# Kernel tuning notes

Hardware: AMD Instinct MI355X
Metric: run time of the kernel (lower is better)

## Reference

```python
import jax, jax.numpy as jnp
import numpy as np
import math

# config constants (from init_kwargs)
W_ROSE, W_QUALITY, W_VOLUME = 0.5, 0.3, 0.2
EPS = 1e-8
DEGEN_EPS = 1e-8


def _rose_score(v):
    # v: [N, n, d] -> [N]; centroid-based radial cosine rose score
    n = v.shape[-2]
    centroid = v.mean(axis=-2, keepdims=True)
    radial = v - centroid
    norms = jnp.clip(jnp.linalg.norm(radial, axis=-1, keepdims=True), EPS)
    u = radial / norms
    cos = jnp.einsum('...id,...jd->...ij', u, u)            # [N, n, n]
    diag = jnp.einsum('...ii->...', cos)
    cos_mean = (cos.sum(axis=(-1, -2)) - diag) / (n * (n - 1))  # off-diagonal mean
    return (cos_mean + 1.0) * 0.5


def _pairwise_sq_dists(v):
    diff = v[..., :, None, :] - v[..., None, :, :]
    return jnp.sum(diff * diff, axis=-1)                    # [N, n, n]


def _regularity(v):
    # SimplexQuality regularity: min_edge / max_edge (1.0 for a regular simplex)
    n = v.shape[-2]
    d = jnp.sqrt(jnp.clip(_pairwise_sq_dists(v), 1e-12))
    off = ~np.eye(n, dtype=bool)                            # static boolean mask
    edges = d[..., off]                                     # [N, n*(n-1)]
    return edges.min(axis=-1) / jnp.clip(edges.max(axis=-1), EPS)


def _cayley_menger_volume(v):
    # v: [N, n, d]; k-simplex with k = n-1; Cayley-Menger determinant volume
    n = v.shape[-2]
    k = n - 1
    d2 = _pairwise_sq_dists(v)                              # [N, n, n]
    bs = d2.shape[:-2]
    top = jnp.concatenate([jnp.zeros(bs + (1, 1), d2.dtype),
                           jnp.ones(bs + (1, n), d2.dtype)], axis=-1)
    bot = jnp.concatenate([jnp.ones(bs + (n, 1), d2.dtype), d2], axis=-1)
    cm = jnp.concatenate([top, bot], axis=-2)               # [N, n+1, n+1]
    det = jnp.linalg.det(cm)
    coeff = ((-1.0) ** (k + 1)) / (2.0 ** k * float(math.factorial(k)) ** 2)
    v2 = coeff * det
    vol = jnp.sqrt(jnp.clip(v2, 0.0))
    is_degenerate = vol < DEGEN_EPS
    return vol, is_degenerate


def setup_inputs() -> dict:
    key = jax.random.key(0)
    k1, k2 = jax.random.split(key)
    B, O, K1, D = 16, 8192, 5, 64
    n_samples = int(O * 0.25)  # 2048
    predicted_simplices = jax.random.normal(k1, (B, O, K1, D), dtype=jnp.float32)
    sample_indices = jax.random.randint(k2, (B, n_samples), 0, O, dtype=jnp.int32)
    return {"predicted_simplices": predicted_simplices,
            "sample_indices": sample_indices}


def reference(predicted_simplices, sample_indices):
    B, O, K1, D = predicted_simplices.shape
    n_samples = sample_indices.shape[1]
    # per-batch gather of sampled simplices (replaces torch per-batch loop)
    sampled = predicted_simplices[jnp.arange(B)[:, None], sample_indices]  # [B, S, K1, D]
    flat = sampled.reshape(B * n_samples, K1, D)

    rose = _rose_score(flat)
    rose_loss = (1.0 - rose).mean()

    regularity = _regularity(flat)
    quality_loss = (1.0 - regularity).mean()

    vol, is_degenerate = _cayley_menger_volume(flat)
    volume_loss = is_degenerate.astype(flat.dtype).mean()

    total_loss = W_ROSE * rose_loss + W_QUALITY * quality_loss + W_VOLUME * volume_loss
    return total_loss
```

## Files before the change

### kernel.cpp

```cpp
#include <hip/hip_runtime.h>

#define K1 5
#define DIM 64
#define OCNT 8192
#define NSAMP_PER_B 2048
#define BLOCK 256
#define LANES_PER_SIMPLEX 16

__device__ __forceinline__ double det4(const double m[4][4]) {
    double c01 = m[2][0] * m[3][1] - m[2][1] * m[3][0];
    double c02 = m[2][0] * m[3][2] - m[2][2] * m[3][0];
    double c03 = m[2][0] * m[3][3] - m[2][3] * m[3][0];
    double c12 = m[2][1] * m[3][2] - m[2][2] * m[3][1];
    double c13 = m[2][1] * m[3][3] - m[2][3] * m[3][1];
    double c23 = m[2][2] * m[3][3] - m[2][3] * m[3][2];
    double d0 = m[1][1] * c23 - m[1][2] * c13 + m[1][3] * c12;
    double d1 = m[1][0] * c23 - m[1][2] * c03 + m[1][3] * c02;
    double d2 = m[1][0] * c13 - m[1][1] * c03 + m[1][3] * c01;
    double d3 = m[1][0] * c12 - m[1][1] * c02 + m[1][2] * c01;
    return m[0][0] * d0 - m[0][1] * d1 + m[0][2] * d2 - m[0][3] * d3;
}

__global__ __launch_bounds__(BLOCK) void cm_main_kernel(
        const float* __restrict__ pts,
        const int* __restrict__ sidx,
        float* __restrict__ block_sums) {
    const int tid = blockIdx.x * BLOCK + threadIdx.x;
    const int t = tid >> 4;
    const int g = threadIdx.x & 15;
    const int b = t >> 11;
    const int o = sidx[t];
    const float* base =
        pts + ((size_t)b * OCNT + (size_t)o) * (K1 * DIM) + g * 4;

    float4 x[K1];
#pragma unroll
    for (int i = 0; i < K1; ++i)
        x[i] = *reinterpret_cast<const float4*>(base + i * DIM);

    float acc[15];
    {
        int k = 0;
#pragma unroll
        for (int i = 0; i < K1; ++i)
#pragma unroll
            for (int j = i; j < K1; ++j) {
                acc[k] = x[i].x * x[j].x + x[i].y * x[j].y +
                         x[i].z * x[j].z + x[i].w * x[j].w;
                ++k;
            }
    }
#pragma unroll
    for (int mask = 1; mask < LANES_PER_SIMPLEX; mask <<= 1) {
#pragma unroll
        for (int k = 0; k < 15; ++k)
            acc[k] += __shfl_xor(acc[k], mask, 64);
    }

    float G[K1][K1];
    {
        int k = 0;
#pragma unroll
        for (int i = 0; i < K1; ++i)
#pragma unroll
            for (int j = i; j < K1; ++j) {
                G[i][j] = acc[k];
                G[j][i] = acc[k];
                ++k;
            }
    }

    float S[K1];
    float T = 0.0f;
#pragma unroll
    for (int i = 0; i < K1; ++i) {
        S[i] = G[i][0] + G[i][1] + G[i][2] + G[i][3] + G[i][4];
        T += S[i];
    }
    float ci[K1];
#pragma unroll
    for (int i = 0; i < K1; ++i) ci[i] = S[i] * 0.2f;
    const float cc = T * 0.04f;

    float nrm[K1];
#pragma unroll
    for (int i = 0; i < K1; ++i) {
        float r2 = G[i][i] - 2.0f * ci[i] + cc;
        r2 = fmaxf(r2, 0.0f);
        nrm[i] = fmaxf(sqrtf(r2), 1e-8f);
    }
    float sumcos = 0.0f;
#pragma unroll
    for (int i = 0; i < K1; ++i)
#pragma unroll
        for (int j = i + 1; j < K1; ++j) {
            float num = G[i][j] - ci[i] - ci[j] + cc;
            sumcos += num / (nrm[i] * nrm[j]);
        }
    const float rose = (sumcos * 0.1f + 1.0f) * 0.5f;

    float dmin = 3.4e38f, dmax = 0.0f;
#pragma unroll
    for (int i = 0; i < K1; ++i)
#pragma unroll
        for (int j = i + 1; j < K1; ++j) {
            float d2 = G[i][i] + G[j][j] - 2.0f * G[i][j];
            float dd = sqrtf(fmaxf(d2, 1e-12f));
            dmin = fminf(dmin, dd);
            dmax = fmaxf(dmax, dd);
        }
    const float reg = dmin / fmaxf(dmax, 1e-8f);

    double W[4][4];
#pragma unroll
    for (int a = 1; a < K1; ++a)
#pragma unroll
        for (int c = 1; c < K1; ++c)
            W[a - 1][c - 1] =
                (double)G[a][c] - (double)G[a][0] - (double)G[0][c] + (double)G[0][0];
    double dW = det4(W);
    double vol = sqrt(fmax(dW, 0.0)) * (1.0 / 24.0);
    const float degen = (vol < 1e-8) ? 1.0f : 0.0f;

    float loss = 0.5f * (1.0f - rose) + 0.3f * (1.0f - reg) + 0.2f * degen;

    loss = (g == 0) ? loss : 0.0f;
#pragma unroll
    for (int off = 32; off > 0; off >>= 1)
        loss += __shfl_down(loss, off, 64);

    __shared__ float wsum[BLOCK / 64];
    const int lane = threadIdx.x & 63;
    const int wave = threadIdx.x >> 6;
    if (lane == 0) wsum[wave] = loss;
    __syncthreads();
    if (threadIdx.x == 0) {
        float s = 0.0f;
#pragma unroll
        for (int w = 0; w < BLOCK / 64; ++w) s += wsum[w];
        block_sums[blockIdx.x] = s;
    }
}

__global__ __launch_bounds__(BLOCK) void cm_final_kernel(
        const float* __restrict__ block_sums, float* __restrict__ out,
        int nblocks, float inv_n) {
    float v = 0.0f;
    for (int i = threadIdx.x; i < nblocks; i += BLOCK) v += block_sums[i];
#pragma unroll
    for (int off = 32; off > 0; off >>= 1)
        v += __shfl_down(v, off, 64);
    __shared__ float wsum[BLOCK / 64];
    const int lane = threadIdx.x & 63;
    const int wave = threadIdx.x >> 6;
    if (lane == 0) wsum[wave] = v;
    __syncthreads();
    if (threadIdx.x == 0) {
        float s = 0.0f;
#pragma unroll
        for (int w = 0; w < BLOCK / 64; ++w) s += wsum[w];
        out[0] = s * inv_n;
    }
}

extern "C" void kernel_launch(void* const* d_in, const int* in_sizes, int n_in,
                              void* d_out, int out_size, void* d_ws, size_t ws_size,
                              hipStream_t stream) {
    const float* pts = (const float*)d_in[0];
    const int* sidx  = (const int*)d_in[1];
    float* out = (float*)d_out;
    float* block_sums = (float*)d_ws;

    const int nsimp = in_sizes[1];
    const int nblocks = nsimp * LANES_PER_SIMPLEX / BLOCK;

    cm_main_kernel<<<nblocks, BLOCK, 0, stream>>>(pts, sidx, block_sums);
    cm_final_kernel<<<1, BLOCK, 0, stream>>>(block_sums, out, nblocks,
                                             1.0f / (float)nsimp);
}
```

Baseline: 209.3 us.

## Use 4 lanes per simplex and compute scalar epilogue once via shared memory

Each simplex is now handled by 4 lanes instead of 16, with every lane loading 16 floats per vertex. This cuts the cross-lane shuffle reduction of the 15 Gram entries from 4 stages to 2. The reduced Gram matrices are written to shared memory, and one wave then runs the scalar epilogue once per simplex (rose, regularity and the double-precision 4x4 determinant) instead of repeating it on every lane. The cost is fewer blocks, more registers per thread, a block-wide barrier, and three idle waves during the epilogue.

```diff
diff --git a/kernel.cpp b/kernel.cpp
--- a/kernel.cpp
+++ b/kernel.cpp
@@ -3,9 +3,9 @@
 #define K1 5
 #define DIM 64
 #define OCNT 8192
-#define NSAMP_PER_B 2048
 #define BLOCK 256
-#define LANES_PER_SIMPLEX 16
+#define LPS 4
+#define SPB (BLOCK / LPS)
 
 __device__ __forceinline__ double det4(const double m[4][4]) {
     double c01 = m[2][0] * m[3][1] - m[2][1] * m[3][0];
@@ -25,18 +25,20 @@
         const float* __restrict__ pts,
         const int* __restrict__ sidx,
         float* __restrict__ block_sums) {
-    const int tid = blockIdx.x * BLOCK + threadIdx.x;
-    const int t = tid >> 4;
-    const int g = threadIdx.x & 15;
+    const int g = threadIdx.x & (LPS - 1);
+    const int s_local = threadIdx.x / LPS;
+    const int t = blockIdx.x * SPB + s_local;
     const int b = t >> 11;
     const int o = sidx[t];
     const float* base =
-        pts + ((size_t)b * OCNT + (size_t)o) * (K1 * DIM) + g * 4;
+        pts + ((size_t)b * OCNT + (size_t)o) * (K1 * DIM) + g * 16;
 
-    float4 x[K1];
+    float4 x[K1][4];
 #pragma unroll
     for (int i = 0; i < K1; ++i)
-        x[i] = *reinterpret_cast<const float4*>(base + i * DIM);
+#pragma unroll
+        for (int q = 0; q < 4; ++q)
+            x[i][q] = *reinterpret_cast<const float4*>(base + i * DIM + q * 4);
 
     float acc[15];
     {
@@ -45,100 +47,104 @@
         for (int i = 0; i < K1; ++i)
 #pragma unroll
             for (int j = i; j < K1; ++j) {
-                acc[k] = x[i].x * x[j].x + x[i].y * x[j].y +
-                         x[i].z * x[j].z + x[i].w * x[j].w;
-                ++k;
+                float s = 0.0f;
+#pragma unroll
+                for (int q = 0; q < 4; ++q) {
+                    s = fmaf(x[i][q].x, x[j][q].x, s);
+                    s = fmaf(x[i][q].y, x[j][q].y, s);
+                    s = fmaf(x[i][q].z, x[j][q].z, s);
+                    s = fmaf(x[i][q].w, x[j][q].w, s);
+                }
+                acc[k++] = s;
             }
     }
 #pragma unroll
-    for (int mask = 1; mask < LANES_PER_SIMPLEX; mask <<= 1) {
+    for (int mask = 1; mask < LPS; mask <<= 1) {
 #pragma unroll
         for (int k = 0; k < 15; ++k)
             acc[k] += __shfl_xor(acc[k], mask, 64);
     }
 
-    float G[K1][K1];
-    {
-        int k = 0;
+    __shared__ float gram[SPB * 15];
+    if (g == 0) {
+#pragma unroll
+        for (int k = 0; k < 15; ++k) gram[s_local * 15 + k] = acc[k];
+    }
+    __syncthreads();
+
+    if (threadIdx.x < SPB) {
+        const float* gp = gram + threadIdx.x * 15;
+        float G[K1][K1];
+        {
+            int k = 0;
+#pragma unroll
+            for (int i = 0; i < K1; ++i)
+#pragma unroll
+                for (int j = i; j < K1; ++j) {
+                    float v = gp[k++];
+                    G[i][j] = v;
+                    G[j][i] = v;
+                }
+        }
+
+        float S[K1];
+        float T = 0.0f;
+#pragma unroll
+        for (int i = 0; i < K1; ++i) {
+            S[i] = G[i][0] + G[i][1] + G[i][2] + G[i][3] + G[i][4];
+            T += S[i];
+        }
+        float ci[K1];
+#pragma unroll
+        for (int i = 0; i < K1; ++i) ci[i] = S[i] * 0.2f;
+        const float cc = T * 0.04f;
+
+        float nrm[K1];
+#pragma unroll
+        for (int i = 0; i < K1; ++i) {
+            float r2 = G[i][i] - 2.0f * ci[i] + cc;
+            r2 = fmaxf(r2, 0.0f);
+            nrm[i] = fmaxf(sqrtf(r2), 1e-8f);
+        }
+        float sumcos = 0.0f;
 #pragma unroll
         for (int i = 0; i < K1; ++i)
 #pragma unroll
-            for (int j = i; j < K1; ++j) {
-                G[i][j] = acc[k];
-                G[j][i] = acc[k];
-                ++k;
+            for (int j = i + 1; j < K1; ++j) {
+                float num = G[i][j] - ci[i] - ci[j] + cc;
+                sumcos += num / (nrm[i] * nrm[j]);
             }
-    }
+        const float rose = (sumcos * 0.1f + 1.0f) * 0.5f;
 
-    float S[K1];
-    float T = 0.0f;
+        float dmin = 3.4e38f, dmax = 0.0f;
 #pragma unroll
-    for (int i = 0; i < K1; ++i) {
-        S[i] = G[i][0] + G[i][1] + G[i][2] + G[i][3] + G[i][4];
-        T += S[i];
-    }
-    float ci[K1];
+        for (int i = 0; i < K1; ++i)
 #pragma unroll
-    for (int i = 0; i < K1; ++i) ci[i] = S[i] * 0.2f;
-    const float cc = T * 0.04f;
+            for (int j = i + 1; j < K1; ++j) {
+                float d2 = G[i][i] + G[j][j] - 2.0f * G[i][j];
+                float dd = sqrtf(fmaxf(d2, 1e-12f));
+                dmin = fminf(dmin, dd);
+                dmax = fmaxf(dmax, dd);
+            }
+        const float reg = dmin / fmaxf(dmax, 1e-8f);
 
-    float nrm[K1];
+        double W[4][4];
 #pragma unroll
-    for (int i = 0; i < K1; ++i) {
-        float r2 = G[i][i] - 2.0f * ci[i] + cc;
-        r2 = fmaxf(r2, 0.0f);
-        nrm[i] = fmaxf(sqrtf(r2), 1e-8f);
-    }
-    float sumcos = 0.0f;
+        for (int a = 1; a < K1; ++a)
 #pragma unroll
-    for (int i = 0; i < K1; ++i)
+            for (int c = 1; c < K1; ++c)
+                W[a - 1][c - 1] = (double)G[a][c] - (double)G[a][0] -
+                                  (double)G[0][c] + (double)G[0][0];
+        double dW = det4(W);
+        double vol = sqrt(fmax(dW, 0.0)) * (1.0 / 24.0);
+        const float degen = (vol < 1e-8) ? 1.0f : 0.0f;
+
+        float loss = 0.5f * (1.0f - rose) + 0.3f * (1.0f - reg) + 0.2f * degen;
+
 #pragma unroll
-        for (int j = i + 1; j < K1; ++j) {
-            float num = G[i][j] - ci[i] - ci[j] + cc;
-            sumcos += num / (nrm[i] * nrm[j]);
-        }
-    const float rose = (sumcos * 0.1f + 1.0f) * 0.5f;
-
-    float dmin = 3.4e38f, dmax = 0.0f;
-#pragma unroll
-    for (int i = 0; i < K1; ++i)
-#pragma unroll
-        for (int j = i + 1; j < K1; ++j) {
-            float d2 = G[i][i] + G[j][j] - 2.0f * G[i][j];
-            float dd = sqrtf(fmaxf(d2, 1e-12f));
-            dmin = fminf(dmin, dd);
-            dmax = fmaxf(dmax, dd);
-        }
-    const float reg = dmin / fmaxf(dmax, 1e-8f);
-
-    double W[4][4];
-#pragma unroll
-    for (int a = 1; a < K1; ++a)
-#pragma unroll
-        for (int c = 1; c < K1; ++c)
-            W[a - 1][c - 1] =
-                (double)G[a][c] - (double)G[a][0] - (double)G[0][c] + (double)G[0][0];
-    double dW = det4(W);
-    double vol = sqrt(fmax(dW, 0.0)) * (1.0 / 24.0);
-    const float degen = (vol < 1e-8) ? 1.0f : 0.0f;
-
-    float loss = 0.5f * (1.0f - rose) + 0.3f * (1.0f - reg) + 0.2f * degen;
-
-    loss = (g == 0) ? loss : 0.0f;
-#pragma unroll
-    for (int off = 32; off > 0; off >>= 1)
-        loss += __shfl_down(loss, off, 64);
-
-    __shared__ float wsum[BLOCK / 64];
-    const int lane = threadIdx.x & 63;
-    const int wave = threadIdx.x >> 6;
-    if (lane == 0) wsum[wave] = loss;
-    __syncthreads();
-    if (threadIdx.x == 0) {
-        float s = 0.0f;
-#pragma unroll
-        for (int w = 0; w < BLOCK / 64; ++w) s += wsum[w];
-        block_sums[blockIdx.x] = s;
+        for (int off = 32; off > 0; off >>= 1)
+            loss += __shfl_down(loss, off, 64);
+        if (threadIdx.x == 0) block_sums[blockIdx.x] = loss;
     }
 }
 
@@ -172,7 +178,7 @@
     float* block_sums = (float*)d_ws;
 
     const int nsimp = in_sizes[1];
-    const int nblocks = nsimp * LANES_PER_SIMPLEX / BLOCK;
+    const int nblocks = nsimp / SPB;
 
     cm_main_kernel<<<nblocks, BLOCK, 0, stream>>>(pts, sidx, block_sums);
     cm_final_kernel<<<1, BLOCK, 0, stream>>>(block_sums, out, nblocks,
```

Measured after the change: 211.0 us. Within noise of the previous version (+0.8%).
